# Kernel optimization log

Measured on AMD Instinct MI355X. Metric: run time of the kernel, lower is better.

Reference implementation:

```python
import jax, jax.numpy as jnp
import numpy as np

N_GRID = 16      # reservoir_n
CHANNELS = 4
R = 2            # receptive-field radius -> 5x5 kernel
T_STEPS = 8
NEG_SLOPE = 0.1


def _extract_patches(S):
    # S: [b, C, n, n] -> patches [b, C, 5, 5, n, n] (kernel offsets u,v)
    Sp = jnp.pad(S, ((0, 0), (0, 0), (R, R), (R, R)))
    k = 2 * R + 1
    rows = [jnp.stack([Sp[:, :, du:du + N_GRID, dv:dv + N_GRID] for dv in range(k)], axis=2)
            for du in range(k)]
    return jnp.stack(rows, axis=2)  # [b, C, k, k, n, n]


def _reservoir_step(S, W):
    # W: [n, n, C_out, C_in, k, k]; per-pixel unique weights (locally connected)
    patches = _extract_patches(S)                       # [b, c, u, v, y, x]
    out = jnp.einsum('bcuvyx,yxocuv->boyx', patches, W)  # [b, C, n, n]
    return jnp.where(out > 0, out, NEG_SLOPE * out)      # leaky_relu(0.1)


def setup_inputs() -> dict:
    key = jax.random.key(0)
    k1, k2 = jax.random.split(key)
    x = jax.random.normal(k1, (8192, 784), dtype=jnp.float32)
    # scale weights down so the T-step recurrence stays numerically tame
    W = jax.random.normal(k2, (N_GRID, N_GRID, CHANNELS, CHANNELS, 2 * R + 1, 2 * R + 1),
                          dtype=jnp.float32) * 0.05
    return {"x": x, "W": W}


def reference(x, W):
    batch = x.shape[0]
    total = N_GRID * N_GRID * CHANNELS  # 1024
    padded = jnp.pad(x, ((0, 0), (0, total - x.shape[1])))
    S = padded.reshape(batch, CHANNELS, N_GRID, N_GRID)
    for _ in range(T_STEPS):
        S = _reservoir_step(S, W)
    S_pooled = S.mean(axis=1)                 # pool over channels -> [b, n, n]
    return S_pooled.reshape(batch, -1)        # [b, n*n]
```

## Files before the change

kernel.cpp:

```cpp
#include <hip/hip_runtime.h>

#define NG 16
#define NC 4
#define BPB 8
#define TSTEPS 8
#define PITCH 34
#define CROW (NG * PITCH)

__device__ __forceinline__ void fma4(float w, const float4& s, float4& a) {
    a.x = fmaf(w, s.x, a.x);
    a.y = fmaf(w, s.y, a.y);
    a.z = fmaf(w, s.z, a.z);
    a.w = fmaf(w, s.w, a.w);
}

__device__ __forceinline__ float4 lrelu4(float4 v) {
    float4 r;
    r.x = fmaxf(v.x, 0.1f * v.x);
    r.y = fmaxf(v.y, 0.1f * v.y);
    r.z = fmaxf(v.z, 0.1f * v.z);
    r.w = fmaxf(v.w, 0.1f * v.w);
    return r;
}

template<int CTRL>
__device__ __forceinline__ float dppf(float x) {
    return __int_as_float(__builtin_amdgcn_update_dpp(
        0, __float_as_int(x), CTRL, 0xF, 0xF, true));
}
template<int CTRL>
__device__ __forceinline__ float4 dpp4(float4 v) {
    float4 r;
    r.x = dppf<CTRL>(v.x);
    r.y = dppf<CTRL>(v.y);
    r.z = dppf<CTRL>(v.z);
    r.w = dppf<CTRL>(v.w);
    return r;
}

__global__ void wt_transpose(const float* __restrict__ W, float4* __restrict__ Wt) {
    int t = blockIdx.x * 256 + threadIdx.x;
    if (t >= 25600) return;
    int r = t >> 8;
    int pix = t & 255;
    int c = r / 25, uv = r - c * 25, u = uv / 5, v = uv - u * 5;
    int y = pix >> 4, x = pix & 15;
    float4 w = make_float4(0.f, 0.f, 0.f, 0.f);
    if ((unsigned)(y + u - 2) < 16u && (unsigned)(x + v - 2) < 16u) {
        int base = pix * 400 + c * 25 + uv;
        w.x = W[base];
        w.y = W[base + 100];
        w.z = W[base + 200];
        w.w = W[base + 300];
    }
    Wt[r * 256 + pix] = w;
}

__global__ __launch_bounds__(512, 8)
void reservoir_kernel(const float* __restrict__ X, const float4* __restrict__ Wt,
                      float* __restrict__ out, int batch) {
    __shared__ float4 smv[NC * CROW];
    float* smf = reinterpret_cast<float*>(smv);

    const int tid = threadIdx.x;
    const int bh  = tid >> 8;
    const int pix = tid & 255;
    const int y = pix >> 4;
    const int x = pix & 15;
    const long itemBase = (long)blockIdx.x * BPB;

    for (int b = 0; b < BPB; ++b) {
        long item = itemBase + b;
        #pragma unroll
        for (int k = 0; k < 2; ++k) {
            int idx = tid + k * 512;
            float v = 0.f;
            if (idx < 784 && item < batch)
                v = __builtin_nontemporal_load(&X[item * 784 + idx]);
            int c = idx >> 8, rem = idx & 255, yy = rem >> 4, xx = rem & 15;
            int phys = (b >> 2) ^ ((xx >> 2) & 1);
            smf[((c * NG + yy) * PITCH + xx * 2 + phys) * 4 + (b & 3)] = v;
        }
    }

    const int swx = (x >> 2) & 1;
    const int xq  = x * 2 + (bh ^ swx);

    const float4* Wp = Wt + pix;
    float4 w0 = Wp[0], w1 = Wp[256], w2 = Wp[512], w3 = Wp[768], w4 = Wp[1024];
    int wnext = 1280;

    __syncthreads();

    #pragma unroll 1
    for (int t = 0; t < TSTEPS; ++t) {
        float4 a0 = {0,0,0,0}, a1 = {0,0,0,0}, a2 = {0,0,0,0}, a3 = {0,0,0,0};

        #pragma unroll 1
        for (int c = 0; c < NC; ++c) {
            const int cb = c * CROW;
            #pragma unroll 1
            for (int u = 0; u < 5; ++u) {
                int yy = y + u - 2;
                yy = yy < 0 ? 0 : (yy > 15 ? 15 : yy);
                const float4 s = smv[cb + yy * PITCH + xq];

                fma4(w2.x, s, a0); fma4(w2.y, s, a1);
                fma4(w2.z, s, a2); fma4(w2.w, s, a3);
                { const float4 tp = dpp4<0x111>(s);
                  fma4(w1.x, tp, a0); fma4(w1.y, tp, a1);
                  fma4(w1.z, tp, a2); fma4(w1.w, tp, a3); }
                { const float4 tp = dpp4<0x101>(s);
                  fma4(w3.x, tp, a0); fma4(w3.y, tp, a1);
                  fma4(w3.z, tp, a2); fma4(w3.w, tp, a3); }
                { const float4 tp = dpp4<0x112>(s);
                  fma4(w0.x, tp, a0); fma4(w0.y, tp, a1);
                  fma4(w0.z, tp, a2); fma4(w0.w, tp, a3); }
                { const float4 tp = dpp4<0x102>(s);
                  fma4(w4.x, tp, a0); fma4(w4.y, tp, a1);
                  fma4(w4.z, tp, a2); fma4(w4.w, tp, a3); }

                __builtin_amdgcn_sched_barrier(0);
                w0 = Wp[wnext];
                w1 = Wp[wnext + 256];
                w2 = Wp[wnext + 512];
                w3 = Wp[wnext + 768];
                w4 = Wp[wnext + 1024];
                wnext += 1280;
                if (wnext >= 25600) wnext = 0;
            }
        }

        a0 = lrelu4(a0); a1 = lrelu4(a1); a2 = lrelu4(a2); a3 = lrelu4(a3);

        if (t < TSTEPS - 1) {
            __syncthreads();
            const int pa = y * PITCH + x * 2 + (bh ^ swx);
            smv[0 * CROW + pa] = a0;
            smv[1 * CROW + pa] = a1;
            smv[2 * CROW + pa] = a2;
            smv[3 * CROW + pa] = a3;
            __syncthreads();
        } else {
            float4 p;
            p.x = (a0.x + a1.x + a2.x + a3.x) * 0.25f;
            p.y = (a0.y + a1.y + a2.y + a3.y) * 0.25f;
            p.z = (a0.z + a1.z + a2.z + a3.z) * 0.25f;
            p.w = (a0.w + a1.w + a2.w + a3.w) * 0.25f;
            const long b0 = itemBase + bh * 4;
            const long ob = b0 * 256 + pix;
            if (b0 + 0 < batch) __builtin_nontemporal_store(p.x, &out[ob + 0 * 256]);
            if (b0 + 1 < batch) __builtin_nontemporal_store(p.y, &out[ob + 1 * 256]);
            if (b0 + 2 < batch) __builtin_nontemporal_store(p.z, &out[ob + 2 * 256]);
            if (b0 + 3 < batch) __builtin_nontemporal_store(p.w, &out[ob + 3 * 256]);
        }
    }
}

extern "C" void kernel_launch(void* const* d_in, const int* in_sizes, int n_in,
                              void* d_out, int out_size, void* d_ws, size_t ws_size,
                              hipStream_t stream) {
    const float* X = (const float*)d_in[0];
    const float* W = (const float*)d_in[1];
    float* out = (float*)d_out;
    const int batch = in_sizes[0] / 784;
    const int blocks = (batch + BPB - 1) / BPB;

    wt_transpose<<<100, 256, 0, stream>>>(W, (float4*)d_ws);
    reservoir_kernel<<<blocks, 512, 0, stream>>>(
        X, (const float4*)d_ws, out, batch);
}
```

Measured before the change: 266.1 us.

## Process 16 batch items per thread to quadruple weight reuse

Each thread now computes its pixel for 16 batch items, held as four float4 groups, instead of 4, with 256-thread blocks covering 16 items. This amortizes every per-pixel weight load from global memory over four times more FMAs. The shared-memory layout moves to a 64-pitch row with an XOR swizzle over four slots. The cost is many more accumulator registers, 64 KB of LDS per block and far fewer resident waves, which reduces latency hiding.

```diff
diff --git a/kernel.cpp b/kernel.cpp
--- a/kernel.cpp
+++ b/kernel.cpp
@@ -2,9 +2,9 @@
 
 #define NG 16
 #define NC 4
-#define BPB 8
+#define BPB 16
 #define TSTEPS 8
-#define PITCH 34
+#define PITCH 64
 #define CROW (NG * PITCH)
 
 __device__ __forceinline__ void fma4(float w, const float4& s, float4& a) {
@@ -56,69 +56,74 @@
     Wt[r * 256 + pix] = w;
 }
 
-__global__ __launch_bounds__(512, 8)
+__global__ __launch_bounds__(256, 2)
 void reservoir_kernel(const float* __restrict__ X, const float4* __restrict__ Wt,
                       float* __restrict__ out, int batch) {
     __shared__ float4 smv[NC * CROW];
     float* smf = reinterpret_cast<float*>(smv);
 
     const int tid = threadIdx.x;
-    const int bh  = tid >> 8;
-    const int pix = tid & 255;
-    const int y = pix >> 4;
-    const int x = pix & 15;
+    const int y = tid >> 4;
+    const int x = tid & 15;
     const long itemBase = (long)blockIdx.x * BPB;
+
+    const int sw = (x >> 1) & 3;
+    const int xb = x << 2;
 
     for (int b = 0; b < BPB; ++b) {
         long item = itemBase + b;
         #pragma unroll
-        for (int k = 0; k < 2; ++k) {
-            int idx = tid + k * 512;
+        for (int k = 0; k < 4; ++k) {
+            int idx = tid + k * 256;
             float v = 0.f;
             if (idx < 784 && item < batch)
                 v = __builtin_nontemporal_load(&X[item * 784 + idx]);
             int c = idx >> 8, rem = idx & 255, yy = rem >> 4, xx = rem & 15;
-            int phys = (b >> 2) ^ ((xx >> 2) & 1);
-            smf[((c * NG + yy) * PITCH + xx * 2 + phys) * 4 + (b & 3)] = v;
+            int phys = (b >> 2) ^ ((xx >> 1) & 3);
+            smf[(((c * NG + yy) << 6) + (xx << 2) + phys) * 4 + (b & 3)] = v;
         }
     }
 
-    const int swx = (x >> 2) & 1;
-    const int xq  = x * 2 + (bh ^ swx);
-
-    const float4* Wp = Wt + pix;
+    const float4* Wp = Wt + tid;
     float4 w0 = Wp[0], w1 = Wp[256], w2 = Wp[512], w3 = Wp[768], w4 = Wp[1024];
     int wnext = 1280;
 
     __syncthreads();
 
+#define TAPQ(WV, T, Q) \
+    fma4(WV.x, T, a0##Q); fma4(WV.y, T, a1##Q); \
+    fma4(WV.z, T, a2##Q); fma4(WV.w, T, a3##Q);
+
+#define QBLOCK(SQ, Q) { \
+    TAPQ(w2, SQ, Q) \
+    { const float4 tp = dpp4<0x111>(SQ); TAPQ(w1, tp, Q) } \
+    { const float4 tp = dpp4<0x101>(SQ); TAPQ(w3, tp, Q) } \
+    { const float4 tp = dpp4<0x112>(SQ); TAPQ(w0, tp, Q) } \
+    { const float4 tp = dpp4<0x102>(SQ); TAPQ(w4, tp, Q) } }
+
     #pragma unroll 1
     for (int t = 0; t < TSTEPS; ++t) {
-        float4 a0 = {0,0,0,0}, a1 = {0,0,0,0}, a2 = {0,0,0,0}, a3 = {0,0,0,0};
+        float4 a00 = {0,0,0,0}, a01 = {0,0,0,0}, a02 = {0,0,0,0}, a03 = {0,0,0,0};
+        float4 a10 = {0,0,0,0}, a11 = {0,0,0,0}, a12 = {0,0,0,0}, a13 = {0,0,0,0};
+        float4 a20 = {0,0,0,0}, a21 = {0,0,0,0}, a22 = {0,0,0,0}, a23 = {0,0,0,0};
+        float4 a30 = {0,0,0,0}, a31 = {0,0,0,0}, a32 = {0,0,0,0}, a33 = {0,0,0,0};
 
         #pragma unroll 1
         for (int c = 0; c < NC; ++c) {
-            const int cb = c * CROW;
             #pragma unroll 1
             for (int u = 0; u < 5; ++u) {
                 int yy = y + u - 2;
                 yy = yy < 0 ? 0 : (yy > 15 ? 15 : yy);
-                const float4 s = smv[cb + yy * PITCH + xq];
-
-                fma4(w2.x, s, a0); fma4(w2.y, s, a1);
-                fma4(w2.z, s, a2); fma4(w2.w, s, a3);
-                { const float4 tp = dpp4<0x111>(s);
-                  fma4(w1.x, tp, a0); fma4(w1.y, tp, a1);
-                  fma4(w1.z, tp, a2); fma4(w1.w, tp, a3); }
-                { const float4 tp = dpp4<0x101>(s);
-                  fma4(w3.x, tp, a0); fma4(w3.y, tp, a1);
-                  fma4(w3.z, tp, a2); fma4(w3.w, tp, a3); }
-                { const float4 tp = dpp4<0x112>(s);
-                  fma4(w0.x, tp, a0); fma4(w0.y, tp, a1);
-                  fma4(w0.z, tp, a2); fma4(w0.w, tp, a3); }
-                { const float4 tp = dpp4<0x102>(s);
-                  fma4(w4.x, tp, a0); fma4(w4.y, tp, a1);
-                  fma4(w4.z, tp, a2); fma4(w4.w, tp, a3); }
+                const int rb = ((c * NG + yy) << 6) + xb;
+                const float4 s0 = smv[rb + (0 ^ sw)];
+                const float4 s1 = smv[rb + (1 ^ sw)];
+                const float4 s2 = smv[rb + (2 ^ sw)];
+                const float4 s3 = smv[rb + (3 ^ sw)];
+
+                QBLOCK(s0, 0)
+                QBLOCK(s1, 1)
+                QBLOCK(s2, 2)
+                QBLOCK(s3, 3)
 
                 __builtin_amdgcn_sched_barrier(0);
                 w0 = Wp[wnext];
@@ -131,28 +136,66 @@
             }
         }
 
-        a0 = lrelu4(a0); a1 = lrelu4(a1); a2 = lrelu4(a2); a3 = lrelu4(a3);
+        a00 = lrelu4(a00); a01 = lrelu4(a01); a02 = lrelu4(a02); a03 = lrelu4(a03);
+        a10 = lrelu4(a10); a11 = lrelu4(a11); a12 = lrelu4(a12); a13 = lrelu4(a13);
+        a20 = lrelu4(a20); a21 = lrelu4(a21); a22 = lrelu4(a22); a23 = lrelu4(a23);
+        a30 = lrelu4(a30); a31 = lrelu4(a31); a32 = lrelu4(a32); a33 = lrelu4(a33);
 
         if (t < TSTEPS - 1) {
             __syncthreads();
-            const int pa = y * PITCH + x * 2 + (bh ^ swx);
-            smv[0 * CROW + pa] = a0;
-            smv[1 * CROW + pa] = a1;
-            smv[2 * CROW + pa] = a2;
-            smv[3 * CROW + pa] = a3;
+            const int pb = (y << 6) + xb;
+            smv[(0 * NG << 6) + pb + (0 ^ sw)] = a00;
+            smv[(0 * NG << 6) + pb + (1 ^ sw)] = a01;
+            smv[(0 * NG << 6) + pb + (2 ^ sw)] = a02;
+            smv[(0 * NG << 6) + pb + (3 ^ sw)] = a03;
+            smv[(1 * NG << 6) + pb + (0 ^ sw)] = a10;
+            smv[(1 * NG << 6) + pb + (1 ^ sw)] = a11;
+            smv[(1 * NG << 6) + pb + (2 ^ sw)] = a12;
+            smv[(1 * NG << 6) + pb + (3 ^ sw)] = a13;
+            smv[(2 * NG << 6) + pb + (0 ^ sw)] = a20;
+            smv[(2 * NG << 6) + pb + (1 ^ sw)] = a21;
+            smv[(2 * NG << 6) + pb + (2 ^ sw)] = a22;
+            smv[(2 * NG << 6) + pb + (3 ^ sw)] = a23;
+            smv[(3 * NG << 6) + pb + (0 ^ sw)] = a30;
+            smv[(3 * NG << 6) + pb + (1 ^ sw)] = a31;
+            smv[(3 * NG << 6) + pb + (2 ^ sw)] = a32;
+            smv[(3 * NG << 6) + pb + (3 ^ sw)] = a33;
             __syncthreads();
         } else {
-            float4 p;
-            p.x = (a0.x + a1.x + a2.x + a3.x) * 0.25f;
-            p.y = (a0.y + a1.y + a2.y + a3.y) * 0.25f;
-            p.z = (a0.z + a1.z + a2.z + a3.z) * 0.25f;
-            p.w = (a0.w + a1.w + a2.w + a3.w) * 0.25f;
-            const long b0 = itemBase + bh * 4;
-            const long ob = b0 * 256 + pix;
-            if (b0 + 0 < batch) __builtin_nontemporal_store(p.x, &out[ob + 0 * 256]);
-            if (b0 + 1 < batch) __builtin_nontemporal_store(p.y, &out[ob + 1 * 256]);
-            if (b0 + 2 < batch) __builtin_nontemporal_store(p.z, &out[ob + 2 * 256]);
-            if (b0 + 3 < batch) __builtin_nontemporal_store(p.w, &out[ob + 3 * 256]);
+            float4 p0, p1, p2, p3;
+            p0.x = (a00.x + a10.x + a20.x + a30.x) * 0.25f;
+            p0.y = (a00.y + a10.y + a20.y + a30.y) * 0.25f;
+            p0.z = (a00.z + a10.z + a20.z + a30.z) * 0.25f;
+            p0.w = (a00.w + a10.w + a20.w + a30.w) * 0.25f;
+            p1.x = (a01.x + a11.x + a21.x + a31.x) * 0.25f;
+            p1.y = (a01.y + a11.y + a21.y + a31.y) * 0.25f;
+            p1.z = (a01.z + a11.z + a21.z + a31.z) * 0.25f;
+            p1.w = (a01.w + a11.w + a21.w + a31.w) * 0.25f;
+            p2.x = (a02.x + a12.x + a22.x + a32.x) * 0.25f;
+            p2.y = (a02.y + a12.y + a22.y + a32.y) * 0.25f;
+            p2.z = (a02.z + a12.z + a22.z + a32.z) * 0.25f;
+            p2.w = (a02.w + a12.w + a22.w + a32.w) * 0.25f;
+            p3.x = (a03.x + a13.x + a23.x + a33.x) * 0.25f;
+            p3.y = (a03.y + a13.y + a23.y + a33.y) * 0.25f;
+            p3.z = (a03.z + a13.z + a23.z + a33.z) * 0.25f;
+            p3.w = (a03.w + a13.w + a23.w + a33.w) * 0.25f;
+            const long ob = itemBase * 256 + tid;
+            if (itemBase + 0  < batch) __builtin_nontemporal_store(p0.x, &out[ob + 0  * 256]);
+            if (itemBase + 1  < batch) __builtin_nontemporal_store(p0.y, &out[ob + 1  * 256]);
+            if (itemBase + 2  < batch) __builtin_nontemporal_store(p0.z, &out[ob + 2  * 256]);
+            if (itemBase + 3  < batch) __builtin_nontemporal_store(p0.w, &out[ob + 3  * 256]);
+            if (itemBase + 4  < batch) __builtin_nontemporal_store(p1.x, &out[ob + 4  * 256]);
+            if (itemBase + 5  < batch) __builtin_nontemporal_store(p1.y, &out[ob + 5  * 256]);
+            if (itemBase + 6  < batch) __builtin_nontemporal_store(p1.z, &out[ob + 6  * 256]);
+            if (itemBase + 7  < batch) __builtin_nontemporal_store(p1.w, &out[ob + 7  * 256]);
+            if (itemBase + 8  < batch) __builtin_nontemporal_store(p2.x, &out[ob + 8  * 256]);
+            if (itemBase + 9  < batch) __builtin_nontemporal_store(p2.y, &out[ob + 9  * 256]);
+            if (itemBase + 10 < batch) __builtin_nontemporal_store(p2.z, &out[ob + 10 * 256]);
+            if (itemBase + 11 < batch) __builtin_nontemporal_store(p2.w, &out[ob + 11 * 256]);
+            if (itemBase + 12 < batch) __builtin_nontemporal_store(p3.x, &out[ob + 12 * 256]);
+            if (itemBase + 13 < batch) __builtin_nontemporal_store(p3.y, &out[ob + 13 * 256]);
+            if (itemBase + 14 < batch) __builtin_nontemporal_store(p3.z, &out[ob + 14 * 256]);
+            if (itemBase + 15 < batch) __builtin_nontemporal_store(p3.w, &out[ob + 15 * 256]);
         }
     }
 }
@@ -167,6 +210,6 @@
     const int blocks = (batch + BPB - 1) / BPB;
 
     wt_transpose<<<100, 256, 0, stream>>>(W, (float4*)d_ws);
-    reservoir_kernel<<<blocks, 512, 0, stream>>>(
+    reservoir_kernel<<<blocks, 256, 0, stream>>>(
         X, (const float4*)d_ws, out, batch);
 }
```

After: 214.1 us. -19.5%, faster.

## Process 16 batch items per block with 8 items per thread to reuse weights

Applied to the files above, without the earlier changes.

Each block now handles 16 batch items instead of 8, and each thread computes two float4 batch groups (8 items), so every weight load from global memory feeds twice as many FMAs. The shared-memory layout moves to a pitch of 64 with a 4-way XOR swizzle to keep the two float4 reads per row conflict-free. Weight reloads for the next (c,u) step are interleaved between tap groups instead of sitting behind a sched barrier. This doubles accumulator registers and shared memory per block, and occupancy is reduced via launch bounds, which could limit latency hiding.

```diff
diff --git a/kernel.cpp b/kernel.cpp
--- a/kernel.cpp
+++ b/kernel.cpp
@@ -2,9 +2,9 @@
 
 #define NG 16
 #define NC 4
-#define BPB 8
+#define BPB 16
 #define TSTEPS 8
-#define PITCH 34
+#define PITCH 64
 #define CROW (NG * PITCH)
 
 __device__ __forceinline__ void fma4(float w, const float4& s, float4& a) {
@@ -56,18 +56,23 @@
     Wt[r * 256 + pix] = w;
 }
 
-__global__ __launch_bounds__(512, 8)
+__global__ __launch_bounds__(512, 4)
 void reservoir_kernel(const float* __restrict__ X, const float4* __restrict__ Wt,
                       float* __restrict__ out, int batch) {
     __shared__ float4 smv[NC * CROW];
     float* smf = reinterpret_cast<float*>(smv);
 
     const int tid = threadIdx.x;
-    const int bh  = tid >> 8;
+    const int oct = tid >> 8;
     const int pix = tid & 255;
     const int y = pix >> 4;
     const int x = pix & 15;
     const long itemBase = (long)blockIdx.x * BPB;
+
+    const int sw = (x >> 1) & 3;
+    const int xb = x << 2;
+    const int q0 = (2 * oct) ^ sw;
+    const int q1 = (2 * oct + 1) ^ sw;
 
     for (int b = 0; b < BPB; ++b) {
         long item = itemBase + b;
@@ -78,13 +83,10 @@
             if (idx < 784 && item < batch)
                 v = __builtin_nontemporal_load(&X[item * 784 + idx]);
             int c = idx >> 8, rem = idx & 255, yy = rem >> 4, xx = rem & 15;
-            int phys = (b >> 2) ^ ((xx >> 2) & 1);
-            smf[((c * NG + yy) * PITCH + xx * 2 + phys) * 4 + (b & 3)] = v;
+            int phys = (b >> 2) ^ ((xx >> 1) & 3);
+            smf[(((c * NG + yy) << 6) + (xx << 2) + phys) * 4 + (b & 3)] = v;
         }
     }
-
-    const int swx = (x >> 2) & 1;
-    const int xq  = x * 2 + (bh ^ swx);
 
     const float4* Wp = Wt + pix;
     float4 w0 = Wp[0], w1 = Wp[256], w2 = Wp[512], w3 = Wp[768], w4 = Wp[1024];
@@ -92,67 +94,82 @@
 
     __syncthreads();
 
+#define TAP(WV, T0, T1) \
+    fma4(WV.x, T0, a00); fma4(WV.x, T1, a01); \
+    fma4(WV.y, T0, a10); fma4(WV.y, T1, a11); \
+    fma4(WV.z, T0, a20); fma4(WV.z, T1, a21); \
+    fma4(WV.w, T0, a30); fma4(WV.w, T1, a31);
+
     #pragma unroll 1
     for (int t = 0; t < TSTEPS; ++t) {
-        float4 a0 = {0,0,0,0}, a1 = {0,0,0,0}, a2 = {0,0,0,0}, a3 = {0,0,0,0};
+        float4 a00 = {0,0,0,0}, a01 = {0,0,0,0};
+        float4 a10 = {0,0,0,0}, a11 = {0,0,0,0};
+        float4 a20 = {0,0,0,0}, a21 = {0,0,0,0};
+        float4 a30 = {0,0,0,0}, a31 = {0,0,0,0};
 
         #pragma unroll 1
         for (int c = 0; c < NC; ++c) {
-            const int cb = c * CROW;
             #pragma unroll 1
             for (int u = 0; u < 5; ++u) {
                 int yy = y + u - 2;
                 yy = yy < 0 ? 0 : (yy > 15 ? 15 : yy);
-                const float4 s = smv[cb + yy * PITCH + xq];
+                const int rb = ((c * NG + yy) << 6) + xb;
+                const float4 s0 = smv[rb + q0];
+                const float4 s1 = smv[rb + q1];
 
-                fma4(w2.x, s, a0); fma4(w2.y, s, a1);
-                fma4(w2.z, s, a2); fma4(w2.w, s, a3);
-                { const float4 tp = dpp4<0x111>(s);
-                  fma4(w1.x, tp, a0); fma4(w1.y, tp, a1);
-                  fma4(w1.z, tp, a2); fma4(w1.w, tp, a3); }
-                { const float4 tp = dpp4<0x101>(s);
-                  fma4(w3.x, tp, a0); fma4(w3.y, tp, a1);
-                  fma4(w3.z, tp, a2); fma4(w3.w, tp, a3); }
-                { const float4 tp = dpp4<0x112>(s);
-                  fma4(w0.x, tp, a0); fma4(w0.y, tp, a1);
-                  fma4(w0.z, tp, a2); fma4(w0.w, tp, a3); }
-                { const float4 tp = dpp4<0x102>(s);
-                  fma4(w4.x, tp, a0); fma4(w4.y, tp, a1);
-                  fma4(w4.z, tp, a2); fma4(w4.w, tp, a3); }
+                TAP(w2, s0, s1)
+                w2 = Wp[wnext + 512];
+                { const float4 t0 = dpp4<0x111>(s0), t1 = dpp4<0x111>(s1);
+                  TAP(w1, t0, t1) }
+                w1 = Wp[wnext + 256];
+                { const float4 t0 = dpp4<0x101>(s0), t1 = dpp4<0x101>(s1);
+                  TAP(w3, t0, t1) }
+                w3 = Wp[wnext + 768];
+                { const float4 t0 = dpp4<0x112>(s0), t1 = dpp4<0x112>(s1);
+                  TAP(w0, t0, t1) }
+                w0 = Wp[wnext];
+                { const float4 t0 = dpp4<0x102>(s0), t1 = dpp4<0x102>(s1);
+                  TAP(w4, t0, t1) }
+                w4 = Wp[wnext + 1024];
 
-                __builtin_amdgcn_sched_barrier(0);
-                w0 = Wp[wnext];
-                w1 = Wp[wnext + 256];
-                w2 = Wp[wnext + 512];
-                w3 = Wp[wnext + 768];
-                w4 = Wp[wnext + 1024];
                 wnext += 1280;
                 if (wnext >= 25600) wnext = 0;
             }
         }
 
-        a0 = lrelu4(a0); a1 = lrelu4(a1); a2 = lrelu4(a2); a3 = lrelu4(a3);
+        a00 = lrelu4(a00); a01 = lrelu4(a01);
+        a10 = lrelu4(a10); a11 = lrelu4(a11);
+        a20 = lrelu4(a20); a21 = lrelu4(a21);
+        a30 = lrelu4(a30); a31 = lrelu4(a31);
 
         if (t < TSTEPS - 1) {
             __syncthreads();
-            const int pa = y * PITCH + x * 2 + (bh ^ swx);
-            smv[0 * CROW + pa] = a0;
-            smv[1 * CROW + pa] = a1;
-            smv[2 * CROW + pa] = a2;
-            smv[3 * CROW + pa] = a3;
+            const int pb = (y << 6) + xb;
+            smv[0 * CROW + pb + q0] = a00;  smv[0 * CROW + pb + q1] = a01;
+            smv[1 * CROW + pb + q0] = a10;  smv[1 * CROW + pb + q1] = a11;
+            smv[2 * CROW + pb + q0] = a20;  smv[2 * CROW + pb + q1] = a21;
+            smv[3 * CROW + pb + q0] = a30;  smv[3 * CROW + pb + q1] = a31;
             __syncthreads();
         } else {
-            float4 p;
-            p.x = (a0.x + a1.x + a2.x + a3.x) * 0.25f;
-            p.y = (a0.y + a1.y + a2.y + a3.y) * 0.25f;
-            p.z = (a0.z + a1.z + a2.z + a3.z) * 0.25f;
-            p.w = (a0.w + a1.w + a2.w + a3.w) * 0.25f;
-            const long b0 = itemBase + bh * 4;
+            float4 p0, p1;
+            p0.x = (a00.x + a10.x + a20.x + a30.x) * 0.25f;
+            p0.y = (a00.y + a10.y + a20.y + a30.y) * 0.25f;
+            p0.z = (a00.z + a10.z + a20.z + a30.z) * 0.25f;
+            p0.w = (a00.w + a10.w + a20.w + a30.w) * 0.25f;
+            p1.x = (a01.x + a11.x + a21.x + a31.x) * 0.25f;
+            p1.y = (a01.y + a11.y + a21.y + a31.y) * 0.25f;
+            p1.z = (a01.z + a11.z + a21.z + a31.z) * 0.25f;
+            p1.w = (a01.w + a11.w + a21.w + a31.w) * 0.25f;
+            const long b0 = itemBase + 8 * oct;
             const long ob = b0 * 256 + pix;
-            if (b0 + 0 < batch) __builtin_nontemporal_store(p.x, &out[ob + 0 * 256]);
-            if (b0 + 1 < batch) __builtin_nontemporal_store(p.y, &out[ob + 1 * 256]);
-            if (b0 + 2 < batch) __builtin_nontemporal_store(p.z, &out[ob + 2 * 256]);
-            if (b0 + 3 < batch) __builtin_nontemporal_store(p.w, &out[ob + 3 * 256]);
+            if (b0 + 0 < batch) __builtin_nontemporal_store(p0.x, &out[ob + 0 * 256]);
+            if (b0 + 1 < batch) __builtin_nontemporal_store(p0.y, &out[ob + 1 * 256]);
+            if (b0 + 2 < batch) __builtin_nontemporal_store(p0.z, &out[ob + 2 * 256]);
+            if (b0 + 3 < batch) __builtin_nontemporal_store(p0.w, &out[ob + 3 * 256]);
+            if (b0 + 4 < batch) __builtin_nontemporal_store(p1.x, &out[ob + 4 * 256]);
+            if (b0 + 5 < batch) __builtin_nontemporal_store(p1.y, &out[ob + 5 * 256]);
+            if (b0 + 6 < batch) __builtin_nontemporal_store(p1.z, &out[ob + 6 * 256]);
+            if (b0 + 7 < batch) __builtin_nontemporal_store(p1.w, &out[ob + 7 * 256]);
         }
     }
 }
```

Result: faster. 232.1 us (-12.8%).
